# Optimization experiments

Hardware: AMD Instinct MI355X
Metric: run time of the kernel (lower is better)

Reference implementation:

```python
import jax, jax.numpy as jnp
import numpy as np
from jax import lax

MAX_DISP = 192
DOWNSAMPLE = 4
DEPTH_CH = MAX_DISP // DOWNSAMPLE  # 48


def _grid_sample_zeros(img, xpix, ypix):
    """Bilinear grid_sample, zero padding, align_corners=False semantics.
    img: [B,C,H,W]; xpix/ypix: [Hout,Wout] pixel-space coords."""
    B, C, H, W = img.shape
    x0 = jnp.floor(xpix)
    y0 = jnp.floor(ypix)
    wx1 = xpix - x0
    wy1 = ypix - y0
    wx0 = 1.0 - wx1
    wy0 = 1.0 - wy1

    def gather(yi, xi):
        valid = (xi >= 0) & (xi < W) & (yi >= 0) & (yi < H)
        xc = jnp.clip(xi, 0, W - 1).astype(jnp.int32)
        yc = jnp.clip(yi, 0, H - 1).astype(jnp.int32)
        v = img[:, :, yc, xc]  # [B,C,Hout,Wout]
        return v * valid.astype(img.dtype)

    out = (gather(y0, x0) * (wy0 * wx0)
           + gather(y0, x0 + 1) * (wy0 * wx1)
           + gather(y0 + 1, x0) * (wy1 * wx0)
           + gather(y0 + 1, x0 + 1) * (wy1 * wx1))
    return out


def _cosine_cost(left, right, depth_ch):
    """cost[b,d,h,w] = mean_c(left[b,c,h,w] * right[b,c,h,w-d]) for w>=d else 0."""
    B, C, H, W = left.shape
    rp = jnp.pad(right, ((0, 0), (0, 0), (0, 0), (depth_ch - 1, 0)))

    def body(_, d):
        r = lax.dynamic_slice_in_dim(rp, depth_ch - 1 - d, W, axis=3)
        return None, jnp.mean(left * r, axis=1)  # [B,H,W]; zero pad gives 0 for w<d

    _, cost = lax.scan(body, None, jnp.arange(depth_ch))  # [D,B,H,W]
    return jnp.transpose(cost, (1, 0, 2, 3))


def _shifted_right(right):
    """Faithful replication of the source's grid_sample call, including its
    transposed (y,x) stacking and the 1/channels x-offset."""
    B, C, H, W = right.shape
    y_vals = -1.0 + 2.0 * jnp.arange(H, dtype=jnp.float32) / H   # base_grid_y values
    x_vals = -1.0 + 2.0 * jnp.arange(W, dtype=jnp.float32) / W - 1.0 / C  # base_grid_x - 1/C
    # grid[...,0] = y_vals[j] -> used as x coordinate; grid[...,1] = x_vals[k] -> y coordinate
    xpix = ((y_vals + 1.0) * W - 1.0) / 2.0            # [H], depends on row index j
    ypix = ((x_vals + 1.0) * H - 1.0) / 2.0            # [W], depends on col index k
    xp = jnp.broadcast_to(xpix[:, None], (H, W))
    yp = jnp.broadcast_to(ypix[None, :], (H, W))
    return _grid_sample_zeros(right, xp, yp)


def setup_inputs() -> dict:
    key = jax.random.key(0)
    k1, k2 = jax.random.split(key)
    B, C, H, W = 4, 512, 96, 320
    left = jax.random.normal(k1, (B, C, H, W), dtype=jnp.float32)
    right = jax.random.normal(k2, (B, C, H, W), dtype=jnp.float32)
    return {"left_features": left, "right_features": right}


def reference(left_features, right_features):
    right_shifted = _shifted_right(right_features)
    cost_1 = _cosine_cost(left_features, right_features, DEPTH_CH)
    cost_2 = _cosine_cost(left_features, right_shifted, DEPTH_CH)
    return jnp.concatenate([cost_1, cost_2], axis=1)  # [B, 2*D, H, W]
```

## Files before the change

kernel.cpp:

```cpp
#include <hip/hip_runtime.h>

namespace {
constexpr int Bn = 4, Cn = 512, Hn = 96, Wn = 320, Dch = 48;
constexpr int HWn = Hn * Wn;
constexpr int WCH = 160;
constexpr int NJ = WCH + Dch - 1;
constexpr int NJP = 208;
constexpr int CC = 8;
constexpr int NT = 256;
}

__global__ __launch_bounds__(NT)
void cost_volume_kernel(const float* __restrict__ left,
                        const float* __restrict__ right,
                        float* __restrict__ out) {
  __shared__ float Ls[CC * WCH];
  __shared__ float Rs[CC * NJP];
  __shared__ float RSs[CC * NJP];
  __shared__ float Rcol[CC * Hn];
  __shared__ float f0t[NJP], f1t[NJP];
  __shared__ int   y0t[NJP], y1t[NJP];

  const int tid = threadIdx.x;
  const int wc = blockIdx.x;
  const int h  = blockIdx.y;
  const int b  = blockIdx.z;
  const int w0c = wc * WCH;
  const int wbase = w0c - (Dch - 1);

  const float yv  = -1.0f + 2.0f * (float)h / 96.0f;
  const float xf  = ((yv + 1.0f) * 320.0f - 1.0f) * 0.5f;
  const float x0f = floorf(xf);
  const float wx1 = xf - x0f;
  const float wx0 = 1.0f - wx1;
  const int ix0 = (int)x0f;
  const bool mx0 = (ix0 >= 0) && (ix0 < Wn);
  const bool mx1 = (ix0 + 1 >= 0) && (ix0 + 1 < Wn);

  for (int j = tid; j < NJP; j += NT) {
    float ff0 = 0.f, ff1 = 0.f; int yy0 = 0, yy1 = 0;
    int wg = wbase + j;
    if (j < NJ && wg >= 0) {
      float xv = -1.0f + 2.0f * (float)wg / 320.0f - (1.0f / 512.0f);
      float yf = ((xv + 1.0f) * 96.0f - 1.0f) * 0.5f;
      float y0fl = floorf(yf);
      float wy1 = yf - y0fl;
      float wy0 = 1.0f - wy1;
      int iy0 = (int)y0fl;
      if (iy0 >= 0 && iy0 < Hn)         { ff0 = wy0; yy0 = iy0; }
      if (iy0 + 1 >= 0 && iy0 + 1 < Hn) { ff1 = wy1; yy1 = iy0 + 1; }
    }
    f0t[j] = ff0; f1t[j] = ff1; y0t[j] = yy0; y1t[j] = yy1;
  }
  for (int v = tid; v < CC * Hn; v += NT) Rcol[v] = 0.f;

  const int wpmin = wbase < 0 ? 0 : wbase;
  const int wpmax = wbase + NJ - 1;
  float xvmin = -1.0f + 2.0f * (float)wpmin / 320.0f - (1.0f / 512.0f);
  float yfmin = ((xvmin + 1.0f) * 96.0f - 1.0f) * 0.5f;
  float xvmax = -1.0f + 2.0f * (float)wpmax / 320.0f - (1.0f / 512.0f);
  float yfmax = ((xvmax + 1.0f) * 96.0f - 1.0f) * 0.5f;
  int ylo = (int)floorf(yfmin); if (ylo < 0) ylo = 0;
  int yhi = (int)floorf(yfmax) + 1; if (yhi > Hn - 1) yhi = Hn - 1;
  const int NY = yhi - ylo + 1;

  const int dt = tid / 20;
  const int wt = tid % 20;
  const bool active = tid < 240;
  const int d0 = dt * 4;
  const int wl0 = wt * 8;
  const int rbase = wl0 - d0 + (Dch - 4);

  float acc1[4][8];
  float acc2[4][8];
  #pragma unroll
  for (int j = 0; j < 4; ++j)
    #pragma unroll
    for (int i = 0; i < 8; ++i) { acc1[j][i] = 0.f; acc2[j][i] = 0.f; }

  const int lplane  = (b * Cn) * HWn + h * Wn;
  const int rplane  = (b * Cn) * HWn + h * Wn;
  const int rplane0 = (b * Cn) * HWn;

  for (int c0 = 0; c0 < Cn; c0 += CC) {
    __syncthreads();
    for (int v = tid; v < CC * (WCH / 4); v += NT) {
      int c = v / (WCH / 4);
      int w4 = (v % (WCH / 4)) * 4;
      const float4 val = *reinterpret_cast<const float4*>(
          left + lplane + (c0 + c) * HWn + w0c + w4);
      *reinterpret_cast<float4*>(&Ls[c * WCH + w4]) = val;
    }
    for (int v = tid; v < CC * NJP; v += NT) {
      int c = v / NJP;
      int j = v - c * NJP;
      float val = 0.f;
      int wg = wbase + j;
      if (j < NJ && wg >= 0)
        val = right[rplane + (c0 + c) * HWn + wg];
      Rs[c * NJP + j] = val;
    }
    for (int v = tid; v < CC * NY; v += NT) {
      int c = v / NY;
      int yy = ylo + (v - c * NY);
      const float* rp = right + rplane0 + (c0 + c) * HWn + yy * Wn;
      float a  = mx0 ? rp[ix0]     : 0.f;
      float bb = mx1 ? rp[ix0 + 1] : 0.f;
      Rcol[c * Hn + yy] = wx0 * a + wx1 * bb;
    }
    __syncthreads();
    for (int v = tid; v < CC * NJP; v += NT) {
      int c = v / NJP;
      int j = v - c * NJP;
      float val = f0t[j] * Rcol[c * Hn + y0t[j]] +
                  f1t[j] * Rcol[c * Hn + y1t[j]];
      RSs[c * NJP + j] = val;
    }
    __syncthreads();
    if (active) {
      #pragma unroll
      for (int c = 0; c < CC; ++c) {
        float lv[8], rv[12], sv[12];
        *reinterpret_cast<float4*>(&lv[0]) =
            *reinterpret_cast<const float4*>(&Ls[c * WCH + wl0]);
        *reinterpret_cast<float4*>(&lv[4]) =
            *reinterpret_cast<const float4*>(&Ls[c * WCH + wl0 + 4]);
        const int rb_ = c * NJP + rbase;
        *reinterpret_cast<float4*>(&rv[0]) =
            *reinterpret_cast<const float4*>(&Rs[rb_]);
        *reinterpret_cast<float4*>(&rv[4]) =
            *reinterpret_cast<const float4*>(&Rs[rb_ + 4]);
        *reinterpret_cast<float4*>(&rv[8]) =
            *reinterpret_cast<const float4*>(&Rs[rb_ + 8]);
        *reinterpret_cast<float4*>(&sv[0]) =
            *reinterpret_cast<const float4*>(&RSs[rb_]);
        *reinterpret_cast<float4*>(&sv[4]) =
            *reinterpret_cast<const float4*>(&RSs[rb_ + 4]);
        *reinterpret_cast<float4*>(&sv[8]) =
            *reinterpret_cast<const float4*>(&RSs[rb_ + 8]);
        #pragma unroll
        for (int j = 0; j < 4; ++j)
          #pragma unroll
          for (int i = 0; i < 8; ++i) {
            acc1[j][i] = fmaf(lv[i], rv[i - j + 3], acc1[j][i]);
            acc2[j][i] = fmaf(lv[i], sv[i - j + 3], acc2[j][i]);
          }
      }
    }
  }

  if (active) {
    const float inv = 1.0f / 512.0f;
    #pragma unroll
    for (int j = 0; j < 4; ++j) {
      const int d = d0 + j;
      float4 o0, o1;
      o0.x = acc1[j][0] * inv; o0.y = acc1[j][1] * inv;
      o0.z = acc1[j][2] * inv; o0.w = acc1[j][3] * inv;
      o1.x = acc1[j][4] * inv; o1.y = acc1[j][5] * inv;
      o1.z = acc1[j][6] * inv; o1.w = acc1[j][7] * inv;
      int oidx = ((b * 96 + d) * Hn + h) * Wn + w0c + wl0;
      *reinterpret_cast<float4*>(out + oidx)     = o0;
      *reinterpret_cast<float4*>(out + oidx + 4) = o1;
      float4 p0, p1;
      p0.x = acc2[j][0] * inv; p0.y = acc2[j][1] * inv;
      p0.z = acc2[j][2] * inv; p0.w = acc2[j][3] * inv;
      p1.x = acc2[j][4] * inv; p1.y = acc2[j][5] * inv;
      p1.z = acc2[j][6] * inv; p1.w = acc2[j][7] * inv;
      int oidx2 = ((b * 96 + (Dch + d)) * Hn + h) * Wn + w0c + wl0;
      *reinterpret_cast<float4*>(out + oidx2)     = p0;
      *reinterpret_cast<float4*>(out + oidx2 + 4) = p1;
    }
  }
}

extern "C" void kernel_launch(void* const* d_in, const int* in_sizes, int n_in,
                              void* d_out, int out_size, void* d_ws, size_t ws_size,
                              hipStream_t stream) {
  const float* left  = (const float*)d_in[0];
  const float* right = (const float*)d_in[1];
  float* out = (float*)d_out;
  (void)in_sizes; (void)n_in; (void)d_ws; (void)ws_size; (void)out_size;
  dim3 grid(2, Hn, Bn);
  dim3 block(NT);
  hipLaunchKernelGGL(cost_volume_kernel, grid, block, 0, stream,
                     left, right, out);
}
```

Baseline: 903.7 us.

## Pack channel pairs to fp16 and use dot2 with larger register tiles

Stores left, right and resampled-right channel pairs as packed fp16 in shared memory and accumulates with v_dot2 fp16-to-fp32 instructions, which halves LDS traffic and the number of multiply-add instructions. Thread tiles grow to 8 disparities by 8 pixels in 128-thread blocks, shared-memory indices are XOR-swizzled to avoid bank conflicts, and the column interpolation for the next channel chunk is double-buffered. Converting inputs to fp16 loses precision across the 512-channel reduction, and the larger accumulator arrays raise register pressure.

```diff
diff --git a/kernel.cpp b/kernel.cpp
--- a/kernel.cpp
+++ b/kernel.cpp
@@ -1,25 +1,54 @@
 #include <hip/hip_runtime.h>
+#include <stdint.h>
+
+typedef __fp16 f16x2 __attribute__((ext_vector_type(2)));
+
+#ifndef __has_builtin
+#define __has_builtin(x) 0
+#endif
 
 namespace {
 constexpr int Bn = 4, Cn = 512, Hn = 96, Wn = 320, Dch = 48;
 constexpr int HWn = Hn * Wn;
 constexpr int WCH = 160;
 constexpr int NJ = WCH + Dch - 1;
-constexpr int NJP = 208;
-constexpr int CC = 8;
-constexpr int NT = 256;
-}
+constexpr int CC = 16;
+constexpr int CP = 8;
+constexpr int NCH = Cn / CC;
+constexpr int QL = 40;
+constexpr int QR = 52;
+constexpr int RSTRIDE = 224;
+constexpr int NT = 128;
+}
+
+__device__ __forceinline__ uint32_t pk2(float a, float b) {
+  f16x2 h = __builtin_amdgcn_cvt_pkrtz(a, b);
+  return __builtin_bit_cast(uint32_t, h);
+}
+
+__device__ __forceinline__ float dot2f(uint32_t a, uint32_t b, float c) {
+#if __has_builtin(__builtin_amdgcn_fdot2)
+  return __builtin_amdgcn_fdot2(__builtin_bit_cast(f16x2, a),
+                                __builtin_bit_cast(f16x2, b), c, false);
+#else
+  f16x2 ha = __builtin_bit_cast(f16x2, a);
+  f16x2 hb = __builtin_bit_cast(f16x2, b);
+  return c + (float)ha.x * (float)hb.x + (float)ha.y * (float)hb.y;
+#endif
+}
+
+__device__ __forceinline__ int swzq(int q) { return q ^ ((q >> 3) & 7); }
 
 __global__ __launch_bounds__(NT)
 void cost_volume_kernel(const float* __restrict__ left,
                         const float* __restrict__ right,
                         float* __restrict__ out) {
-  __shared__ float Ls[CC * WCH];
-  __shared__ float Rs[CC * NJP];
-  __shared__ float RSs[CC * NJP];
-  __shared__ float Rcol[CC * Hn];
-  __shared__ float f0t[NJP], f1t[NJP];
-  __shared__ int   y0t[NJP], y1t[NJP];
+  __shared__ uint32_t Ls[CP * WCH];
+  __shared__ uint32_t Rs[CP * RSTRIDE];
+  __shared__ uint32_t RSs[CP * RSTRIDE];
+  __shared__ float Rcol[2][CC * Hn];
+  __shared__ float f0t[QR * 4], f1t[QR * 4];
+  __shared__ int   y0t[QR * 4], y1t[QR * 4];
 
   const int tid = threadIdx.x;
   const int wc = blockIdx.x;
@@ -37,8 +66,18 @@
   const bool mx0 = (ix0 >= 0) && (ix0 < Wn);
   const bool mx1 = (ix0 + 1 >= 0) && (ix0 + 1 < Wn);
 
-  for (int j = tid; j < NJP; j += NT) {
-    float ff0 = 0.f, ff1 = 0.f; int yy0 = 0, yy1 = 0;
+  const int wpmin = wbase < 0 ? 0 : wbase;
+  const int wpmax = wbase + NJ - 1;
+  float xvmin = -1.0f + 2.0f * (float)wpmin / 320.0f - (1.0f / 512.0f);
+  float yfmin = ((xvmin + 1.0f) * 96.0f - 1.0f) * 0.5f;
+  float xvmax = -1.0f + 2.0f * (float)wpmax / 320.0f - (1.0f / 512.0f);
+  float yfmax = ((xvmax + 1.0f) * 96.0f - 1.0f) * 0.5f;
+  int ylo = (int)floorf(yfmin); if (ylo < 0) ylo = 0;
+  int yhi = (int)floorf(yfmax) + 1; if (yhi > Hn - 1) yhi = Hn - 1;
+  const int NY = yhi - ylo + 1;
+
+  for (int j = tid; j < QR * 4; j += NT) {
+    float ff0 = 0.f, ff1 = 0.f; int yy0 = ylo, yy1 = ylo;
     int wg = wbase + j;
     if (j < NJ && wg >= 0) {
       float xv = -1.0f + 2.0f * (float)wg / 320.0f - (1.0f / 512.0f);
@@ -52,99 +91,115 @@
     }
     f0t[j] = ff0; f1t[j] = ff1; y0t[j] = yy0; y1t[j] = yy1;
   }
-  for (int v = tid; v < CC * Hn; v += NT) Rcol[v] = 0.f;
-
-  const int wpmin = wbase < 0 ? 0 : wbase;
-  const int wpmax = wbase + NJ - 1;
-  float xvmin = -1.0f + 2.0f * (float)wpmin / 320.0f - (1.0f / 512.0f);
-  float yfmin = ((xvmin + 1.0f) * 96.0f - 1.0f) * 0.5f;
-  float xvmax = -1.0f + 2.0f * (float)wpmax / 320.0f - (1.0f / 512.0f);
-  float yfmax = ((xvmax + 1.0f) * 96.0f - 1.0f) * 0.5f;
-  int ylo = (int)floorf(yfmin); if (ylo < 0) ylo = 0;
-  int yhi = (int)floorf(yfmax) + 1; if (yhi > Hn - 1) yhi = Hn - 1;
-  const int NY = yhi - ylo + 1;
-
-  const int dt = tid / 20;
-  const int wt = tid % 20;
-  const bool active = tid < 240;
-  const int d0 = dt * 4;
-  const int wl0 = wt * 8;
-  const int rbase = wl0 - d0 + (Dch - 4);
-
-  float acc1[4][8];
-  float acc2[4][8];
-  #pragma unroll
-  for (int j = 0; j < 4; ++j)
-    #pragma unroll
-    for (int i = 0; i < 8; ++i) { acc1[j][i] = 0.f; acc2[j][i] = 0.f; }
-
-  const int lplane  = (b * Cn) * HWn + h * Wn;
-  const int rplane  = (b * Cn) * HWn + h * Wn;
-  const int rplane0 = (b * Cn) * HWn;
-
-  for (int c0 = 0; c0 < Cn; c0 += CC) {
-    __syncthreads();
-    for (int v = tid; v < CC * (WCH / 4); v += NT) {
-      int c = v / (WCH / 4);
-      int w4 = (v % (WCH / 4)) * 4;
-      const float4 val = *reinterpret_cast<const float4*>(
-          left + lplane + (c0 + c) * HWn + w0c + w4);
-      *reinterpret_cast<float4*>(&Ls[c * WCH + w4]) = val;
-    }
-    for (int v = tid; v < CC * NJP; v += NT) {
-      int c = v / NJP;
-      int j = v - c * NJP;
-      float val = 0.f;
-      int wg = wbase + j;
-      if (j < NJ && wg >= 0)
-        val = right[rplane + (c0 + c) * HWn + wg];
-      Rs[c * NJP + j] = val;
-    }
-    for (int v = tid; v < CC * NY; v += NT) {
-      int c = v / NY;
-      int yy = ylo + (v - c * NY);
-      const float* rp = right + rplane0 + (c0 + c) * HWn + yy * Wn;
+  for (int v = tid; v < 2 * CC * Hn; v += NT)
+    Rcol[v / (CC * Hn)][v % (CC * Hn)] = 0.f;
+  __syncthreads();
+
+  {
+    for (int t = tid; t < CC * NY; t += NT) {
+      int c = t / NY; int yy = ylo + (t - c * NY);
+      const float* rp = right + ((size_t)(b * Cn + c) * Hn + yy) * Wn;
       float a  = mx0 ? rp[ix0]     : 0.f;
       float bb = mx1 ? rp[ix0 + 1] : 0.f;
-      Rcol[c * Hn + yy] = wx0 * a + wx1 * bb;
-    }
+      Rcol[0][c * Hn + yy] = wx0 * a + wx1 * bb;
+    }
+  }
+
+  const int dg = tid / 20;
+  const int wg = tid % 20;
+  const bool active = tid < 120;
+  const int d0 = dg * 8;
+  const int wl0 = wg * 8;
+  const int jb = 8 * (wg - dg) + 40;
+  const int qb = jb >> 2;
+  const int swl0 = swzq(wl0 >> 2) * 4;
+  const int swl1 = swzq((wl0 >> 2) + 1) * 4;
+  int srv[4];
+  #pragma unroll
+  for (int k = 0; k < 4; ++k) srv[k] = swzq(qb + k) * 4;
+
+  float acc1[8][8], acc2[8][8];
+  #pragma unroll
+  for (int jd = 0; jd < 8; ++jd)
+    #pragma unroll
+    for (int i = 0; i < 8; ++i) { acc1[jd][i] = 0.f; acc2[jd][i] = 0.f; }
+
+  for (int ch = 0; ch < NCH; ++ch) {
+    const int c0 = ch * CC;
+    const int cur = ch & 1;
     __syncthreads();
-    for (int v = tid; v < CC * NJP; v += NT) {
-      int c = v / NJP;
-      int j = v - c * NJP;
-      float val = f0t[j] * Rcol[c * Hn + y0t[j]] +
-                  f1t[j] * Rcol[c * Hn + y1t[j]];
-      RSs[c * NJP + j] = val;
+
+    for (int t = tid; t < CP * QL; t += NT) {
+      int cp = t / QL, qw = t - cp * QL;
+      const float* l0 = left + ((size_t)(b * Cn + c0 + 2 * cp) * Hn + h) * Wn + w0c + qw * 4;
+      const float* l1 = l0 + (size_t)HWn;
+      float4 va = *(const float4*)l0;
+      float4 vb = *(const float4*)l1;
+      *(uint4*)&Ls[cp * WCH + swzq(qw) * 4] =
+          make_uint4(pk2(va.x, vb.x), pk2(va.y, vb.y), pk2(va.z, vb.z), pk2(va.w, vb.w));
+    }
+    for (int t = tid; t < CP * QR; t += NT) {
+      int cp = t / QR, q = t - cp * QR;
+      const float* r0 = right + ((size_t)(b * Cn + c0 + 2 * cp) * Hn + h) * Wn;
+      const float* r1 = r0 + (size_t)HWn;
+      uint32_t o[4];
+      #pragma unroll
+      for (int e = 0; e < 4; ++e) {
+        int j = 4 * q + e; int wgl = wbase + j;
+        float a = 0.f, bb = 0.f;
+        if (j < NJ && wgl >= 0) { a = r0[wgl]; bb = r1[wgl]; }
+        o[e] = pk2(a, bb);
+      }
+      *(uint4*)&Rs[cp * RSTRIDE + swzq(q) * 4] = make_uint4(o[0], o[1], o[2], o[3]);
+    }
+    for (int t = tid; t < CP * QR; t += NT) {
+      int cp = t / QR, q = t - cp * QR;
+      const float* rc0 = &Rcol[cur][(2 * cp) * Hn];
+      const float* rc1 = &Rcol[cur][(2 * cp + 1) * Hn];
+      uint32_t o[4];
+      #pragma unroll
+      for (int e = 0; e < 4; ++e) {
+        int j = 4 * q + e;
+        float v0 = f0t[j] * rc0[y0t[j]] + f1t[j] * rc0[y1t[j]];
+        float v1 = f0t[j] * rc1[y0t[j]] + f1t[j] * rc1[y1t[j]];
+        o[e] = pk2(v0, v1);
+      }
+      *(uint4*)&RSs[cp * RSTRIDE + swzq(q) * 4] = make_uint4(o[0], o[1], o[2], o[3]);
+    }
+    if (ch + 1 < NCH) {
+      const int c0n = c0 + CC;
+      for (int t = tid; t < CC * NY; t += NT) {
+        int c = t / NY; int yy = ylo + (t - c * NY);
+        const float* rp = right + ((size_t)(b * Cn + c0n + c) * Hn + yy) * Wn;
+        float a  = mx0 ? rp[ix0]     : 0.f;
+        float bb = mx1 ? rp[ix0 + 1] : 0.f;
+        Rcol[cur ^ 1][c * Hn + yy] = wx0 * a + wx1 * bb;
+      }
     }
     __syncthreads();
+
     if (active) {
       #pragma unroll
-      for (int c = 0; c < CC; ++c) {
-        float lv[8], rv[12], sv[12];
-        *reinterpret_cast<float4*>(&lv[0]) =
-            *reinterpret_cast<const float4*>(&Ls[c * WCH + wl0]);
-        *reinterpret_cast<float4*>(&lv[4]) =
-            *reinterpret_cast<const float4*>(&Ls[c * WCH + wl0 + 4]);
-        const int rb_ = c * NJP + rbase;
-        *reinterpret_cast<float4*>(&rv[0]) =
-            *reinterpret_cast<const float4*>(&Rs[rb_]);
-        *reinterpret_cast<float4*>(&rv[4]) =
-            *reinterpret_cast<const float4*>(&Rs[rb_ + 4]);
-        *reinterpret_cast<float4*>(&rv[8]) =
-            *reinterpret_cast<const float4*>(&Rs[rb_ + 8]);
-        *reinterpret_cast<float4*>(&sv[0]) =
-            *reinterpret_cast<const float4*>(&RSs[rb_]);
-        *reinterpret_cast<float4*>(&sv[4]) =
-            *reinterpret_cast<const float4*>(&RSs[rb_ + 4]);
-        *reinterpret_cast<float4*>(&sv[8]) =
-            *reinterpret_cast<const float4*>(&RSs[rb_ + 8]);
-        #pragma unroll
-        for (int j = 0; j < 4; ++j)
+      for (int cp = 0; cp < CP; ++cp) {
+        uint32_t lv[8], rv[16];
+        *(uint4*)&lv[0] = *(const uint4*)&Ls[cp * WCH + swl0];
+        *(uint4*)&lv[4] = *(const uint4*)&Ls[cp * WCH + swl1];
+        #pragma unroll
+        for (int k = 0; k < 4; ++k)
+          *(uint4*)&rv[4 * k] = *(const uint4*)&Rs[cp * RSTRIDE + srv[k]];
+        #pragma unroll
+        for (int jd = 0; jd < 8; ++jd)
           #pragma unroll
-          for (int i = 0; i < 8; ++i) {
-            acc1[j][i] = fmaf(lv[i], rv[i - j + 3], acc1[j][i]);
-            acc2[j][i] = fmaf(lv[i], sv[i - j + 3], acc2[j][i]);
-          }
+          for (int i = 0; i < 8; ++i)
+            acc1[jd][i] = dot2f(lv[i], rv[i - jd + 7], acc1[jd][i]);
+        #pragma unroll
+        for (int k = 0; k < 4; ++k)
+          *(uint4*)&rv[4 * k] = *(const uint4*)&RSs[cp * RSTRIDE + srv[k]];
+        #pragma unroll
+        for (int jd = 0; jd < 8; ++jd)
+          #pragma unroll
+          for (int i = 0; i < 8; ++i)
+            acc2[jd][i] = dot2f(lv[i], rv[i - jd + 7], acc2[jd][i]);
       }
     }
   }
@@ -152,24 +207,24 @@
   if (active) {
     const float inv = 1.0f / 512.0f;
     #pragma unroll
-    for (int j = 0; j < 4; ++j) {
-      const int d = d0 + j;
+    for (int jd = 0; jd < 8; ++jd) {
+      const int d = d0 + jd;
       float4 o0, o1;
-      o0.x = acc1[j][0] * inv; o0.y = acc1[j][1] * inv;
-      o0.z = acc1[j][2] * inv; o0.w = acc1[j][3] * inv;
-      o1.x = acc1[j][4] * inv; o1.y = acc1[j][5] * inv;
-      o1.z = acc1[j][6] * inv; o1.w = acc1[j][7] * inv;
-      int oidx = ((b * 96 + d) * Hn + h) * Wn + w0c + wl0;
-      *reinterpret_cast<float4*>(out + oidx)     = o0;
-      *reinterpret_cast<float4*>(out + oidx + 4) = o1;
+      o0.x = acc1[jd][0] * inv; o0.y = acc1[jd][1] * inv;
+      o0.z = acc1[jd][2] * inv; o0.w = acc1[jd][3] * inv;
+      o1.x = acc1[jd][4] * inv; o1.y = acc1[jd][5] * inv;
+      o1.z = acc1[jd][6] * inv; o1.w = acc1[jd][7] * inv;
+      size_t oidx = ((size_t)(b * 96 + d) * Hn + h) * Wn + w0c + wl0;
+      *(float4*)(out + oidx)     = o0;
+      *(float4*)(out + oidx + 4) = o1;
       float4 p0, p1;
-      p0.x = acc2[j][0] * inv; p0.y = acc2[j][1] * inv;
-      p0.z = acc2[j][2] * inv; p0.w = acc2[j][3] * inv;
-      p1.x = acc2[j][4] * inv; p1.y = acc2[j][5] * inv;
-      p1.z = acc2[j][6] * inv; p1.w = acc2[j][7] * inv;
-      int oidx2 = ((b * 96 + (Dch + d)) * Hn + h) * Wn + w0c + wl0;
-      *reinterpret_cast<float4*>(out + oidx2)     = p0;
-      *reinterpret_cast<float4*>(out + oidx2 + 4) = p1;
+      p0.x = acc2[jd][0] * inv; p0.y = acc2[jd][1] * inv;
+      p0.z = acc2[jd][2] * inv; p0.w = acc2[jd][3] * inv;
+      p1.x = acc2[jd][4] * inv; p1.y = acc2[jd][5] * inv;
+      p1.z = acc2[jd][6] * inv; p1.w = acc2[jd][7] * inv;
+      size_t oidx2 = ((size_t)(b * 96 + Dch + d) * Hn + h) * Wn + w0c + wl0;
+      *(float4*)(out + oidx2)     = p0;
+      *(float4*)(out + oidx2 + 4) = p1;
     }
   }
 }
@@ -181,7 +236,7 @@
   const float* right = (const float*)d_in[1];
   float* out = (float*)d_out;
   (void)in_sizes; (void)n_in; (void)d_ws; (void)ws_size; (void)out_size;
-  dim3 grid(2, Hn, Bn);
+  dim3 grid(Wn / WCH, Hn, Bn);
   dim3 block(NT);
   hipLaunchKernelGGL(cost_volume_kernel, grid, block, 0, stream,
                      left, right, out);
```

Measured after the change: 841.4 us. -6.9%, faster.
